# Kernel tuning notes

Hardware: AMD Instinct MI355X
Metric: run time of the kernel (lower is better)

Reference implementation:

```python
import jax, jax.numpy as jnp
import numpy as np

B, T, R = 64, 32, 49          # batch, seq_len, num image regions
E = 512                        # embed_size == hidden_size
L = 2                          # num_layers
V = 30000                      # vocab_size


def setup_inputs() -> dict:
    key = jax.random.key(0)
    ks = jax.random.split(key, 8)
    s = 1.0 / np.sqrt(E)  # xavier-ish scale for recurrent weights
    return {
        "features": jax.random.normal(ks[0], (B, R, E), jnp.float32),
        "captions": jax.random.randint(ks[1], (B, T), 0, V),
        "embed_table": jax.random.normal(ks[2], (V, E), jnp.float32) * 0.01,
        "W_ih": jax.random.normal(ks[3], (L, 4 * E, E), jnp.float32) * s,
        "W_hh": jax.random.normal(ks[4], (L, 4 * E, E), jnp.float32) * s,
        "b_ih": jnp.zeros((L, 4 * E), jnp.float32),
        "b_hh": jnp.zeros((L, 4 * E), jnp.float32),
        "W_lin": jax.random.normal(ks[5], (V, 2 * E), jnp.float32) * 0.01,
        "b_lin": jnp.zeros((V,), jnp.float32),
    }


def reference(features, captions, embed_table, W_ih, W_hh, b_ih, b_hh, W_lin, b_lin):
    num_layers = W_ih.shape[0]
    emb = embed_table[captions]                        # [B, T, E]
    mean_f = features.mean(axis=1)                     # [B, E]
    h0 = jnp.stack([mean_f] * num_layers)              # [L, B, H]
    c0 = jnp.stack([mean_f] * num_layers)

    def step(carry, x_t):
        h, c = carry                                   # each [L, B, H]
        inp = x_t                                      # [B, E]
        hs, cs = [], []
        for l in range(num_layers):
            gates = inp @ W_ih[l].T + b_ih[l] + h[l] @ W_hh[l].T + b_hh[l]
            i, f, g, o = jnp.split(gates, 4, axis=-1)  # PyTorch gate order i,f,g,o
            c_new = jax.nn.sigmoid(f) * c[l] + jax.nn.sigmoid(i) * jnp.tanh(g)
            h_new = jax.nn.sigmoid(o) * jnp.tanh(c_new)
            hs.append(h_new)
            cs.append(c_new)
            inp = h_new
        h_top = inp                                    # [B, H]
        # dot attention over image regions
        scores = jnp.einsum('brd,bd->br', features, h_top)
        alpha = jax.nn.softmax(scores, axis=1)
        context = jnp.einsum('br,brd->bd', alpha, features)
        logit = jnp.concatenate([h_top, context], axis=1) @ W_lin.T + b_lin
        return (jnp.stack(hs), jnp.stack(cs)), logit

    _, logits = jax.lax.scan(step, (h0, c0), jnp.swapaxes(emb, 0, 1))  # [T, B, V]
    return jnp.swapaxes(logits, 0, 1)                  # [B, T, V]
```

## Files before the change

### kernel.cpp

```cpp
#include <hip/hip_runtime.h>

#define B_ 64
#define T_ 32
#define R_ 49
#define E_ 512
#define V_ 30000

using bfrag = __attribute__((ext_vector_type(8))) short;
using ffrag = __attribute__((ext_vector_type(4))) float;

__device__ __forceinline__ float bf2f(short u) {
    union { unsigned u32; float f; } x;
    x.u32 = ((unsigned)(unsigned short)u) << 16;
    return x.f;
}
__device__ __forceinline__ unsigned short f2bf(float f) {
    union { float f; unsigned u; } x; x.f = f;
    unsigned r = x.u + 0x7fffu + ((x.u >> 16) & 1u);
    return (unsigned short)(r >> 16);
}
__device__ __forceinline__ float sigm(float x) { return 1.f / (1.f + __expf(-x)); }

#define GLDS(g, l) __builtin_amdgcn_global_load_lds( \
    (const __attribute__((address_space(1))) void*)(g), \
    (__attribute__((address_space(3))) void*)(l), 16, 0, 0)

__global__ __launch_bounds__(256)
void cvt_kernel(const float* __restrict__ src, unsigned short* __restrict__ dst, int n8)
{
    int i = blockIdx.x * 256 + threadIdx.x;
    if (i >= n8) return;
    const float4* s = (const float4*)src + (size_t)i * 2;
    float4 a = s[0], b = s[1];
    bfrag o;
    o[0] = (short)f2bf(a.x); o[1] = (short)f2bf(a.y);
    o[2] = (short)f2bf(a.z); o[3] = (short)f2bf(a.w);
    o[4] = (short)f2bf(b.x); o[5] = (short)f2bf(b.y);
    o[6] = (short)f2bf(b.z); o[7] = (short)f2bf(b.w);
    *(bfrag*)(dst + (size_t)i * 8) = o;
}

__global__ __launch_bounds__(256)
void gemm_bt(const unsigned short* __restrict__ A,
             const unsigned short* __restrict__ W,
             const float* __restrict__ bias1,
             const float* __restrict__ bias2,
             float* __restrict__ outp,
             int M, int N, int K)
{
    __shared__ __align__(16) unsigned short As[128 * 32];
    __shared__ __align__(16) unsigned short Bs[128 * 32];
    const int tid  = threadIdx.x;
    const int wave = tid >> 6, lane = tid & 63;
    const int lrow = lane & 15, kq = lane >> 4;
    const int m0 = blockIdx.x * 128, n0 = blockIdx.y * 128;
    const int wm = (wave >> 1) * 64, wn = (wave & 1) * 64;

    ffrag acc[4][4];
#pragma unroll
    for (int i = 0; i < 4; i++)
#pragma unroll
        for (int j = 0; j < 4; j++) acc[i][j] = ffrag{0.f, 0.f, 0.f, 0.f};

    const int ca = tid, cb = 256 + tid;
    const int ar0 = m0 + (ca >> 2), ar1 = m0 + (cb >> 2);
    const int k8a = (ca & 3) * 8, k8b = (cb & 3) * 8;
    const int wr0 = min(n0 + (ca >> 2), N - 1);
    const int wr1 = min(n0 + (cb >> 2), N - 1);

    unsigned short* ldsA0 = As + (wave * 64) * 8;
    unsigned short* ldsA1 = As + (256 + wave * 64) * 8;
    unsigned short* ldsB0 = Bs + (wave * 64) * 8;
    unsigned short* ldsB1 = Bs + (256 + wave * 64) * 8;

    for (int k0 = 0; k0 < K; k0 += 32) {
        GLDS(A + (size_t)ar0 * K + k0 + k8a, ldsA0);
        GLDS(A + (size_t)ar1 * K + k0 + k8b, ldsA1);
        GLDS(W + (size_t)wr0 * K + k0 + k8a, ldsB0);
        GLDS(W + (size_t)wr1 * K + k0 + k8b, ldsB1);
        __syncthreads();
        bfrag af[4], bw[4];
#pragma unroll
        for (int i = 0; i < 4; i++)
            af[i] = *(const bfrag*)(As + (wm + i * 16 + lrow) * 32 + kq * 8);
#pragma unroll
        for (int j = 0; j < 4; j++)
            bw[j] = *(const bfrag*)(Bs + (wn + j * 16 + lrow) * 32 + kq * 8);
#pragma unroll
        for (int i = 0; i < 4; i++)
#pragma unroll
            for (int j = 0; j < 4; j++)
                acc[i][j] = __builtin_amdgcn_mfma_f32_16x16x32_bf16(af[i], bw[j], acc[i][j], 0, 0, 0);
        __syncthreads();
    }

#pragma unroll
    for (int j = 0; j < 4; j++) {
        int col  = n0 + wn + j * 16 + lrow;
        int colc = min(col, N - 1);
        float bs = 0.f;
        if (bias1) bs += bias1[colc];
        if (bias2) bs += bias2[colc];
        bool ok = (col < N);
#pragma unroll
        for (int i = 0; i < 4; i++) {
            int rbase = m0 + wm + i * 16 + kq * 4;
#pragma unroll
            for (int r = 0; r < 4; r++) {
                float v = acc[i][j][r] + bs;
                if (ok) outp[(size_t)(rbase + r) * N + col] = v;
            }
        }
    }
}

__global__ __launch_bounds__(256)
void lstm_cell(const unsigned short* __restrict__ Wih,
               const unsigned short* __restrict__ Whh,
               const unsigned short* __restrict__ xin,
               const float*          __restrict__ pre,
               const float*          __restrict__ bih,
               const float*          __restrict__ bhh,
               const unsigned short* __restrict__ hprev,
               unsigned short*       __restrict__ hout,
               float*                __restrict__ cst)
{
    const int tid  = threadIdx.x;
    const int wave = tid >> 6, lane = tid & 63;
    const int lrow = lane & 15, kq = lane >> 4;
    const int b0 = (blockIdx.x & 3) * 16;
    const int e0 = (blockIdx.x >> 2) * 16;
    const int wr = wave * 512 + e0 + lrow;

    ffrag acc = {0.f, 0.f, 0.f, 0.f};
    if (xin) {
#pragma unroll
        for (int k0 = 0; k0 < 512; k0 += 32) {
            bfrag a = *(const bfrag*)(xin + (b0 + lrow) * 512 + k0 + kq * 8);
            bfrag w = *(const bfrag*)(Wih + (size_t)wr * 512 + k0 + kq * 8);
            acc = __builtin_amdgcn_mfma_f32_16x16x32_bf16(a, w, acc, 0, 0, 0);
        }
    }
#pragma unroll
    for (int k0 = 0; k0 < 512; k0 += 32) {
        bfrag a = *(const bfrag*)(hprev + (b0 + lrow) * 512 + k0 + kq * 8);
        bfrag w = *(const bfrag*)(Whh + (size_t)wr * 512 + k0 + kq * 8);
        acc = __builtin_amdgcn_mfma_f32_16x16x32_bf16(a, w, acc, 0, 0, 0);
    }

    __shared__ float gb[4][16][17];
#pragma unroll
    for (int r = 0; r < 4; r++) gb[wave][kq * 4 + r][lrow] = acc[r];
    __syncthreads();

    const int m = tid >> 4, el = tid & 15;
    const int b = b0 + m, e = e0 + el;
    float gi = gb[0][m][el], gf = gb[1][m][el], gg = gb[2][m][el], go = gb[3][m][el];
    if (pre) {
        const float* p = pre + (size_t)b * 2048;
        gi += p[e]; gf += p[512 + e]; gg += p[1024 + e]; go += p[1536 + e];
    }
    if (bih) {
        gi += bih[e]        + bhh[e];
        gf += bih[512 + e]  + bhh[512 + e];
        gg += bih[1024 + e] + bhh[1024 + e];
        go += bih[1536 + e] + bhh[1536 + e];
    }
    float cold = cst[(size_t)b * 512 + e];
    float cn = sigm(gf) * cold + sigm(gi) * tanhf(gg);
    float hn = sigm(go) * tanhf(cn);
    cst[(size_t)b * 512 + e]  = cn;
    hout[(size_t)b * 512 + e] = f2bf(hn);
}

__global__ __launch_bounds__(256)
void attn_kernel(const float* __restrict__ features,
                 const unsigned short* __restrict__ Htop,
                 unsigned short* __restrict__ Z)
{
    const int bt = blockIdx.x;
    const int b = bt >> 5, t = bt & 31;
    const unsigned short* h = Htop + ((size_t)(t + 1) * B_ + b) * E_;
    const float* f = features + (size_t)b * R_ * E_;
    const int tid = threadIdx.x, wave = tid >> 6, lane = tid & 63;

    __shared__ float hf[E_];
    __shared__ float sc[64];
    hf[tid]       = bf2f((short)h[tid]);
    hf[256 + tid] = bf2f((short)h[256 + tid]);
    __syncthreads();

    for (int r = wave; r < R_; r += 4) {
        const float4* fr = (const float4*)(f + r * E_ + lane * 8);
        float4 v0 = fr[0], v1 = fr[1];
        const float* hp = hf + lane * 8;
        float s = v0.x * hp[0] + v0.y * hp[1] + v0.z * hp[2] + v0.w * hp[3]
                + v1.x * hp[4] + v1.y * hp[5] + v1.z * hp[6] + v1.w * hp[7];
        for (int off = 32; off; off >>= 1) s += __shfl_down(s, off);
        if (lane == 0) sc[r] = s;
    }
    __syncthreads();
    if (tid < 64) {
        float v = (tid < R_) ? sc[tid] : -3.4e38f;
        float mx = v;
        for (int off = 32; off; off >>= 1) mx = fmaxf(mx, __shfl_xor(mx, off));
        float ex = (tid < R_) ? __expf(v - mx) : 0.f;
        float sum = ex;
        for (int off = 32; off; off >>= 1) sum += __shfl_xor(sum, off);
        if (tid < R_) sc[tid] = ex / sum;
    }
    __syncthreads();

    const int e0 = tid * 2;
    float c0 = 0.f, c1 = 0.f;
    for (int r = 0; r < R_; r++) {
        float a = sc[r];
        c0 += a * f[r * E_ + e0];
        c1 += a * f[r * E_ + e0 + 1];
    }
    unsigned short* zr = Z + (size_t)bt * (2 * E_);
    zr[e0] = h[e0]; zr[e0 + 1] = h[e0 + 1];
    zr[E_ + e0]     = f2bf(c0);
    zr[E_ + e0 + 1] = f2bf(c1);
}

__global__ __launch_bounds__(256)
void init_kernel(const float* __restrict__ features,
                 const int* __restrict__ captions,
                 const float* __restrict__ embed,
                 float* __restrict__ c0, float* __restrict__ c1,
                 unsigned short* __restrict__ H0, unsigned short* __restrict__ Htop,
                 unsigned short* __restrict__ Aemb)
{
    const int blk = blockIdx.x, tid = threadIdx.x;
    if (blk < 128) {
        int g = blk * 256 + tid;
        int b = g >> 9, e = g & 511;
        float s = 0.f;
        for (int r = 0; r < R_; r++) s += features[((size_t)b * R_ + r) * E_ + e];
        float mean = s * (1.f / 49.f);
        c0[g] = mean; c1[g] = mean;
        unsigned short mb = f2bf(mean);
        H0[g] = mb; Htop[g] = mb;
    } else {
        int idx = (blk - 128) * 256 + tid;
        int row = idx >> 6, k8 = (idx & 63) * 8;
        int bb = row & 63, tt = row >> 6;
        int tok = captions[bb * T_ + tt];
        const float4* s = (const float4*)(embed + (size_t)tok * E_ + k8);
        float4 a = s[0], bq = s[1];
        bfrag o;
        o[0] = (short)f2bf(a.x);  o[1] = (short)f2bf(a.y);
        o[2] = (short)f2bf(a.z);  o[3] = (short)f2bf(a.w);
        o[4] = (short)f2bf(bq.x); o[5] = (short)f2bf(bq.y);
        o[6] = (short)f2bf(bq.z); o[7] = (short)f2bf(bq.w);
        *(bfrag*)(Aemb + (size_t)row * E_ + k8) = o;
    }
}

extern "C" void kernel_launch(void* const* d_in, const int* in_sizes, int n_in,
                              void* d_out, int out_size, void* d_ws, size_t ws_size,
                              hipStream_t stream)
{
    const float* features = (const float*)d_in[0];
    const int*   captions = (const int*)d_in[1];
    const float* embed    = (const float*)d_in[2];
    const float* W_ih     = (const float*)d_in[3];
    const float* W_hh     = (const float*)d_in[4];
    const float* b_ih     = (const float*)d_in[5];
    const float* b_hh     = (const float*)d_in[6];
    const float* W_lin    = (const float*)d_in[7];
    const float* b_lin    = (const float*)d_in[8];
    float* out = (float*)d_out;

    char* ws = (char*)d_ws;
    float*          X0     = (float*)(ws);
    unsigned short* H0     = (unsigned short*)(ws + 16777216);
    unsigned short* Htop   = (unsigned short*)(ws + 18939904);
    float*          c0     = (float*)(ws + 21102592);
    float*          c1     = (float*)(ws + 21233664);
    unsigned short* Z      = (unsigned short*)(ws + 21364736);
    unsigned short* Aemb   = (unsigned short*)(ws + 25559040);
    unsigned short* Wb_ih  = (unsigned short*)(ws + 27656192);
    unsigned short* Wb_hh  = (unsigned short*)(ws + 31850496);
    unsigned short* Wb_lin = (unsigned short*)(ws + 36044800);

    const size_t BE = (size_t)B_ * E_;

    cvt_kernel<<<1024, 256, 0, stream>>>(W_ih, Wb_ih, 2 * 2048 * 512 / 8);
    cvt_kernel<<<1024, 256, 0, stream>>>(W_hh, Wb_hh, 2 * 2048 * 512 / 8);
    cvt_kernel<<<15000, 256, 0, stream>>>(W_lin, Wb_lin, V_ * 1024 / 8);

    init_kernel<<<640, 256, 0, stream>>>(features, captions, embed, c0, c1, H0, Htop, Aemb);

    gemm_bt<<<dim3(16, 16), 256, 0, stream>>>(Aemb, Wb_ih, b_ih, b_hh, X0, 2048, 2048, 512);

    for (int t = 0; t < T_; t++) {
        lstm_cell<<<128, 256, 0, stream>>>(nullptr, Wb_hh, nullptr,
                                           X0 + (size_t)t * B_ * 2048,
                                           nullptr, nullptr,
                                           H0 + (size_t)t * BE, H0 + (size_t)(t + 1) * BE, c0);
        lstm_cell<<<128, 256, 0, stream>>>(Wb_ih + 2048 * 512, Wb_hh + 2048 * 512,
                                           H0 + (size_t)(t + 1) * BE,
                                           nullptr, b_ih + 2048, b_hh + 2048,
                                           Htop + (size_t)t * BE, Htop + (size_t)(t + 1) * BE, c1);
    }

    attn_kernel<<<B_ * T_, 256, 0, stream>>>(features, Htop, Z);

    gemm_bt<<<dim3(16, 235), 256, 0, stream>>>(Z, Wb_lin, b_lin, nullptr, out, 2048, V_, 1024);

    (void)in_sizes; (void)n_in; (void)out_size; (void)ws_size;
}
```

Before: 1.135 ms.

## Wavefront-pipeline LSTM layers in one launch and remap GEMM tiles across XCDs

Runs layer 0 at step k and layer 1 at step k-1 together in a single 256-block launch, so the recurrence takes T+1 launches instead of 2T and the two layers work concurrently. The GEMM kernel also remaps block IDs so each group of contiguous tiles lands on the same XCD, which is meant to improve L2 locality. The costs are an extra pipeline step, some idle blocks in the first and last launches, and per-block branching to pick which layer to run.

```diff
diff --git a/kernel.cpp b/kernel.cpp
--- a/kernel.cpp
+++ b/kernel.cpp
@@ -53,7 +53,16 @@
     const int tid  = threadIdx.x;
     const int wave = tid >> 6, lane = tid & 63;
     const int lrow = lane & 15, kq = lane >> 4;
-    const int m0 = blockIdx.x * 128, n0 = blockIdx.y * 128;
+
+    const int gx = gridDim.x;
+    const int nwg = gx * gridDim.y;
+    int bid = blockIdx.y * gx + blockIdx.x;
+    if ((nwg & 7) == 0) {
+        const int cpx = nwg >> 3;
+        bid = (bid & 7) * cpx + (bid >> 3);
+    }
+    const int m0 = (bid % gx) * 128, n0 = (bid / gx) * 128;
+
     const int wm = (wave >> 1) * 64, wn = (wave & 1) * 64;
 
     ffrag acc[4][4];
@@ -115,22 +124,50 @@
 }
 
 __global__ __launch_bounds__(256)
-void lstm_cell(const unsigned short* __restrict__ Wih,
-               const unsigned short* __restrict__ Whh,
-               const unsigned short* __restrict__ xin,
-               const float*          __restrict__ pre,
-               const float*          __restrict__ bih,
-               const float*          __restrict__ bhh,
-               const unsigned short* __restrict__ hprev,
-               unsigned short*       __restrict__ hout,
-               float*                __restrict__ cst)
-{
+void lstm_step(const unsigned short* __restrict__ Wbih,
+               const unsigned short* __restrict__ Wbhh,
+               const float* __restrict__ X0,
+               const float* __restrict__ b_ih,
+               const float* __restrict__ b_hh,
+               unsigned short* __restrict__ H0,
+               unsigned short* __restrict__ Htop,
+               float* __restrict__ c0, float* __restrict__ c1,
+               int t1, int t2)
+{
+    const int layer = blockIdx.x >> 7;
+    const int blk   = blockIdx.x & 127;
     const int tid  = threadIdx.x;
     const int wave = tid >> 6, lane = tid & 63;
     const int lrow = lane & 15, kq = lane >> 4;
-    const int b0 = (blockIdx.x & 3) * 16;
-    const int e0 = (blockIdx.x >> 2) * 16;
+    const int b0 = (blk & 3) * 16;
+    const int e0 = (blk >> 2) * 16;
     const int wr = wave * 512 + e0 + lrow;
+    const size_t BE = (size_t)B_ * E_;
+
+    const unsigned short *xin, *hprev, *Wih, *Whh;
+    const float *pre, *bih, *bhh;
+    unsigned short* hout; float* cst;
+
+    if (layer == 0) {
+        if (t1 < 0) return;
+        xin = nullptr; Wih = nullptr;
+        Whh = Wbhh;
+        pre = X0 + (size_t)t1 * B_ * 2048;
+        bih = nullptr; bhh = nullptr;
+        hprev = H0 + (size_t)t1 * BE;
+        hout  = H0 + (size_t)(t1 + 1) * BE;
+        cst = c0;
+    } else {
+        if (t2 < 0) return;
+        xin = H0 + (size_t)(t2 + 1) * BE;
+        Wih = Wbih + 2048 * 512;
+        Whh = Wbhh + 2048 * 512;
+        pre = nullptr;
+        bih = b_ih + 2048; bhh = b_hh + 2048;
+        hprev = Htop + (size_t)t2 * BE;
+        hout  = Htop + (size_t)(t2 + 1) * BE;
+        cst = c1;
+    }
 
     ffrag acc = {0.f, 0.f, 0.f, 0.f};
     if (xin) {
@@ -285,8 +322,6 @@
     unsigned short* Wb_hh  = (unsigned short*)(ws + 31850496);
     unsigned short* Wb_lin = (unsigned short*)(ws + 36044800);
 
-    const size_t BE = (size_t)B_ * E_;
-
     cvt_kernel<<<1024, 256, 0, stream>>>(W_ih, Wb_ih, 2 * 2048 * 512 / 8);
     cvt_kernel<<<1024, 256, 0, stream>>>(W_hh, Wb_hh, 2 * 2048 * 512 / 8);
     cvt_kernel<<<15000, 256, 0, stream>>>(W_lin, Wb_lin, V_ * 1024 / 8);
@@ -295,15 +330,10 @@
 
     gemm_bt<<<dim3(16, 16), 256, 0, stream>>>(Aemb, Wb_ih, b_ih, b_hh, X0, 2048, 2048, 512);
 
-    for (int t = 0; t < T_; t++) {
-        lstm_cell<<<128, 256, 0, stream>>>(nullptr, Wb_hh, nullptr,
-                                           X0 + (size_t)t * B_ * 2048,
-                                           nullptr, nullptr,
-                                           H0 + (size_t)t * BE, H0 + (size_t)(t + 1) * BE, c0);
-        lstm_cell<<<128, 256, 0, stream>>>(Wb_ih + 2048 * 512, Wb_hh + 2048 * 512,
-                                           H0 + (size_t)(t + 1) * BE,
-                                           nullptr, b_ih + 2048, b_hh + 2048,
-                                           Htop + (size_t)t * BE, Htop + (size_t)(t + 1) * BE, c1);
+    for (int k = 0; k <= T_; k++) {
+        lstm_step<<<256, 256, 0, stream>>>(Wb_ih, Wb_hh, X0, b_ih, b_hh,
+                                           H0, Htop, c0, c1,
+                                           (k < T_) ? k : -1, k - 1);
     }
 
     attn_kernel<<<B_ * T_, 256, 0, stream>>>(features, Htop, Z);
```

After: 943.7 us. 1.2x faster.

## Replace per-step LSTM launches with a persistent cooperative kernel and pipelined layers

Applied to the files above, without the earlier changes.

Replaces 64 separate lstm_cell launches plus the input-projection GEMM with one cooperative persistent kernel of 256 blocks. Each block keeps its weight slice in LDS and its cell state in a register. The two layers run as a wavefront pipeline, with layer 1 one step behind layer 0, separated by grid.sync. This removes launch overhead and repeated weight reloads. In exchange it adds grid-wide barriers, recomputes the layer-0 input projection inside the recurrence, and requires all blocks to be co-resident.

```diff
diff --git a/kernel.cpp b/kernel.cpp
--- a/kernel.cpp
+++ b/kernel.cpp
@@ -1,4 +1,7 @@
 #include <hip/hip_runtime.h>
+#include <hip/hip_cooperative_groups.h>
+
+namespace cg = cooperative_groups;
 
 #define B_ 64
 #define T_ 32
@@ -114,63 +117,96 @@
     }
 }
 
-__global__ __launch_bounds__(256)
-void lstm_cell(const unsigned short* __restrict__ Wih,
-               const unsigned short* __restrict__ Whh,
-               const unsigned short* __restrict__ xin,
-               const float*          __restrict__ pre,
-               const float*          __restrict__ bih,
-               const float*          __restrict__ bhh,
-               const unsigned short* __restrict__ hprev,
-               unsigned short*       __restrict__ hout,
-               float*                __restrict__ cst)
-{
+__global__ __launch_bounds__(256, 1)
+void lstm_persist(const unsigned short* __restrict__ Wbih,
+                  const unsigned short* __restrict__ Wbhh,
+                  const unsigned short* __restrict__ Aemb,
+                  const float* __restrict__ b_ih,
+                  const float* __restrict__ b_hh,
+                  unsigned short* __restrict__ H0,
+                  unsigned short* __restrict__ Htop,
+                  const float* __restrict__ c0,
+                  const float* __restrict__ c1)
+{
+    cg::grid_group grid = cg::this_grid();
+
+    __shared__ __align__(16) unsigned short sW[2 * 4 * 16 * 512];
+    __shared__ float gb[4][16][17];
+
+    const int layer = blockIdx.x >> 7;
+    const int blk   = blockIdx.x & 127;
     const int tid  = threadIdx.x;
     const int wave = tid >> 6, lane = tid & 63;
     const int lrow = lane & 15, kq = lane >> 4;
-    const int b0 = (blockIdx.x & 3) * 16;
-    const int e0 = (blockIdx.x >> 2) * 16;
+    const int b0 = (blk & 3) * 16;
+    const int e0 = (blk >> 2) * 16;
     const int wr = wave * 512 + e0 + lrow;
-
-    ffrag acc = {0.f, 0.f, 0.f, 0.f};
-    if (xin) {
-#pragma unroll
-        for (int k0 = 0; k0 < 512; k0 += 32) {
-            bfrag a = *(const bfrag*)(xin + (b0 + lrow) * 512 + k0 + kq * 8);
-            bfrag w = *(const bfrag*)(Wih + (size_t)wr * 512 + k0 + kq * 8);
-            acc = __builtin_amdgcn_mfma_f32_16x16x32_bf16(a, w, acc, 0, 0, 0);
-        }
-    }
-#pragma unroll
-    for (int k0 = 0; k0 < 512; k0 += 32) {
-        bfrag a = *(const bfrag*)(hprev + (b0 + lrow) * 512 + k0 + kq * 8);
-        bfrag w = *(const bfrag*)(Whh + (size_t)wr * 512 + k0 + kq * 8);
-        acc = __builtin_amdgcn_mfma_f32_16x16x32_bf16(a, w, acc, 0, 0, 0);
-    }
-
-    __shared__ float gb[4][16][17];
-#pragma unroll
-    for (int r = 0; r < 4; r++) gb[wave][kq * 4 + r][lrow] = acc[r];
-    __syncthreads();
+    const size_t BE = (size_t)B_ * E_;
+
+    const unsigned short* Wih = Wbih + (size_t)layer * 2048 * 512;
+    const unsigned short* Whh = Wbhh + (size_t)layer * 2048 * 512;
+
+#pragma unroll
+    for (int it = 0; it < 16; ++it)
+        GLDS(Wih + (size_t)wr * 512 + it * 32 + kq * 8, sW + (size_t)(wave * 16 + it) * 512);
+#pragma unroll
+    for (int it = 0; it < 16; ++it)
+        GLDS(Whh + (size_t)wr * 512 + it * 32 + kq * 8, sW + (size_t)((4 + wave) * 16 + it) * 512);
 
     const int m = tid >> 4, el = tid & 15;
     const int b = b0 + m, e = e0 + el;
-    float gi = gb[0][m][el], gf = gb[1][m][el], gg = gb[2][m][el], go = gb[3][m][el];
-    if (pre) {
-        const float* p = pre + (size_t)b * 2048;
-        gi += p[e]; gf += p[512 + e]; gg += p[1024 + e]; go += p[1536 + e];
-    }
-    if (bih) {
-        gi += bih[e]        + bhh[e];
-        gf += bih[512 + e]  + bhh[512 + e];
-        gg += bih[1024 + e] + bhh[1024 + e];
-        go += bih[1536 + e] + bhh[1536 + e];
-    }
-    float cold = cst[(size_t)b * 512 + e];
-    float cn = sigm(gf) * cold + sigm(gi) * tanhf(gg);
-    float hn = sigm(go) * tanhf(cn);
-    cst[(size_t)b * 512 + e]  = cn;
-    hout[(size_t)b * 512 + e] = f2bf(hn);
+    const float* bih = b_ih + layer * 2048;
+    const float* bhh = b_hh + layer * 2048;
+    const float bi = bih[e]        + bhh[e];
+    const float bf = bih[512 + e]  + bhh[512 + e];
+    const float bg = bih[1024 + e] + bhh[1024 + e];
+    const float bo = bih[1536 + e] + bhh[1536 + e];
+    float creg = (layer ? c1 : c0)[(size_t)b * 512 + e];
+
+    const unsigned short* sWi = sW + (size_t)wave * 16 * 512;
+    const unsigned short* sWh = sW + (size_t)(4 + wave) * 16 * 512;
+
+    __syncthreads();
+
+    for (int k = 0; k <= T_; ++k) {
+        const int t = layer ? (k - 1) : k;
+        if (t >= 0 && t < T_) {
+            const unsigned short* xin   = layer ? (H0 + (size_t)(t + 1) * BE)
+                                                : (Aemb + (size_t)t * BE);
+            const unsigned short* hprev = layer ? (Htop + (size_t)t * BE)
+                                                : (H0 + (size_t)t * BE);
+            unsigned short* hout        = layer ? (Htop + (size_t)(t + 1) * BE)
+                                                : (H0 + (size_t)(t + 1) * BE);
+
+            ffrag acc = {0.f, 0.f, 0.f, 0.f};
+#pragma unroll
+            for (int i = 0; i < 16; ++i) {
+                bfrag a = *(const bfrag*)(xin + (b0 + lrow) * 512 + i * 32 + kq * 8);
+                bfrag w = *(const bfrag*)(sWi + (i * 64 + lane) * 8);
+                acc = __builtin_amdgcn_mfma_f32_16x16x32_bf16(a, w, acc, 0, 0, 0);
+            }
+#pragma unroll
+            for (int i = 0; i < 16; ++i) {
+                bfrag a = *(const bfrag*)(hprev + (b0 + lrow) * 512 + i * 32 + kq * 8);
+                bfrag w = *(const bfrag*)(sWh + (i * 64 + lane) * 8);
+                acc = __builtin_amdgcn_mfma_f32_16x16x32_bf16(a, w, acc, 0, 0, 0);
+            }
+
+#pragma unroll
+            for (int r = 0; r < 4; r++) gb[wave][kq * 4 + r][lrow] = acc[r];
+            __syncthreads();
+
+            float gi = gb[0][m][el] + bi;
+            float gf = gb[1][m][el] + bf;
+            float gg = gb[2][m][el] + bg;
+            float go = gb[3][m][el] + bo;
+            float cn = sigm(gf) * creg + sigm(gi) * tanhf(gg);
+            float hn = sigm(go) * tanhf(cn);
+            creg = cn;
+            hout[(size_t)b * 512 + e] = f2bf(hn);
+        }
+        grid.sync();
+    }
 }
 
 __global__ __launch_bounds__(256)
@@ -274,7 +310,6 @@
     float* out = (float*)d_out;
 
     char* ws = (char*)d_ws;
-    float*          X0     = (float*)(ws);
     unsigned short* H0     = (unsigned short*)(ws + 16777216);
     unsigned short* Htop   = (unsigned short*)(ws + 18939904);
     float*          c0     = (float*)(ws + 21102592);
@@ -285,25 +320,21 @@
     unsigned short* Wb_hh  = (unsigned short*)(ws + 31850496);
     unsigned short* Wb_lin = (unsigned short*)(ws + 36044800);
 
-    const size_t BE = (size_t)B_ * E_;
-
     cvt_kernel<<<1024, 256, 0, stream>>>(W_ih, Wb_ih, 2 * 2048 * 512 / 8);
     cvt_kernel<<<1024, 256, 0, stream>>>(W_hh, Wb_hh, 2 * 2048 * 512 / 8);
     cvt_kernel<<<15000, 256, 0, stream>>>(W_lin, Wb_lin, V_ * 1024 / 8);
 
     init_kernel<<<640, 256, 0, stream>>>(features, captions, embed, c0, c1, H0, Htop, Aemb);
 
-    gemm_bt<<<dim3(16, 16), 256, 0, stream>>>(Aemb, Wb_ih, b_ih, b_hh, X0, 2048, 2048, 512);
-
-    for (int t = 0; t < T_; t++) {
-        lstm_cell<<<128, 256, 0, stream>>>(nullptr, Wb_hh, nullptr,
-                                           X0 + (size_t)t * B_ * 2048,
-                                           nullptr, nullptr,
-                                           H0 + (size_t)t * BE, H0 + (size_t)(t + 1) * BE, c0);
-        lstm_cell<<<128, 256, 0, stream>>>(Wb_ih + 2048 * 512, Wb_hh + 2048 * 512,
-                                           H0 + (size_t)(t + 1) * BE,
-                                           nullptr, b_ih + 2048, b_hh + 2048,
-                                           Htop + (size_t)t * BE, Htop + (size_t)(t + 1) * BE, c1);
+    {
+        const unsigned short* a0 = Wb_ih; const unsigned short* a1 = Wb_hh;
+        const unsigned short* a2 = Aemb;
+        const float* a3 = b_ih; const float* a4 = b_hh;
+        unsigned short* a5 = H0; unsigned short* a6 = Htop;
+        const float* a7 = c0; const float* a8 = c1;
+        void* args[] = { &a0, &a1, &a2, &a3, &a4, &a5, &a6, &a7, &a8 };
+        hipLaunchCooperativeKernel((void*)lstm_persist, dim3(256), dim3(256),
+                                   args, 0, stream);
     }
 
     attn_kernel<<<B_ * T_, 256, 0, stream>>>(features, Htop, Z);
```

After: 1.666 ms. 1.47x slower.
